# Kernel optimization log

Hardware: AMD Instinct MI355X
Metric: run time of the kernel (lower is better)

Reference implementation:

```python
import jax, jax.numpy as jnp
import numpy as np

BS, L, D, ITEM_NUM = 64, 100, 64, 100000  # batch, max_seq_len, embedding_dim, item vocab
NEG_INF = -10000.0


def setup_inputs() -> dict:
    key = jax.random.key(0)
    k1, k2, k3, k4, k5 = jax.random.split(key, 5)
    N = BS * (L + 1)
    return {
        "prec_vec": jax.random.normal(k1, (BS * L, D), jnp.float32),
        "score_embs": jax.random.normal(k2, (N, D), jnp.float32),
        "pop_prob_list": jax.random.uniform(k3, (ITEM_NUM + 1,), jnp.float32, 0.01, 1.0),
        "sample_items_id": jax.random.randint(k4, (N,), 0, ITEM_NUM + 1, dtype=jnp.int32),
        "log_mask": jax.random.randint(k5, (BS, L), 0, 2, dtype=jnp.int32),
    }


def reference(prec_vec, score_embs, pop_prob_list, sample_items_id, log_mask):
    bs, L_ = log_mask.shape
    N = sample_items_id.shape[0]  # bs * (L+1)

    # debiased in-batch sampled-softmax logits: [bs*L, N]
    debias = jnp.log(pop_prob_list[sample_items_id])
    logits = jnp.matmul(prec_vec, score_embs.T) - debias[None, :]

    # column mask: padded positions (log_mask==0); last position of each seq always valid
    col_valid = jnp.concatenate(
        [log_mask, jnp.ones((bs, 1), log_mask.dtype)], axis=1
    ).reshape(-1)  # [N]
    logits = jnp.where(col_valid[None, :] == 0, NEG_INF, logits)

    # duplicate-item mask: dup[i, k] = any item in sequence i equals sample_items_id[k]
    id_list = sample_items_id.reshape(bs, L_ + 1)
    dup = (sample_items_id[None, None, :] == id_list[:, :, None]).any(axis=1)  # [bs, N]

    # targets: label for (i, j) is flat column i*(L+1) + j + 1
    tgt = jnp.arange(bs)[:, None] * (L_ + 1) + jnp.arange(L_)[None, :] + 1  # [bs, L]

    # apply dup mask per (i, j) but never mask the row's own target column
    not_target = jnp.arange(N)[None, None, :] != tgt[:, :, None]  # [bs, L, N]
    mask3 = dup[:, None, :] & not_target
    logits3 = jnp.where(mask3, NEG_INF, logits.reshape(bs, L_, N))

    # masked cross-entropy, mean over valid (log_mask != 0) rows
    logits2 = logits3.reshape(bs * L_, N)
    labels = tgt.reshape(-1)
    logp = jax.nn.log_softmax(logits2, axis=-1)
    nll = -jnp.take_along_axis(logp, labels[:, None], axis=1)[:, 0]  # [bs*L]
    w = (log_mask.reshape(-1) != 0).astype(logits2.dtype)
    return jnp.sum(nll * w) / jnp.sum(w)
```

## Files before the change

kernel.cpp:

```cpp
#include <hip/hip_runtime.h>

#define NEG_INF (-10000.0f)
#define L_SEQ   100
#define N_COLS  6464
#define D_      64
#define N_ROWS  6400
#define NS      16

#define OFF_PS  0
#define OFF_XT  409600

typedef __attribute__((ext_vector_type(8))) short short8;
typedef __attribute__((ext_vector_type(4))) float f32x4;
union F8 { short8 v; unsigned short u[8]; unsigned w[4]; };

__device__ __forceinline__ unsigned short f2bf(float f) {
  unsigned u = __float_as_uint(f);
  return (unsigned short)((u + 0x7FFFu + ((u >> 16) & 1u)) >> 16);
}
__device__ __forceinline__ unsigned packbf(float lo, float hi) {
  return (__float_as_uint(hi) & 0xFFFF0000u) | (__float_as_uint(lo) >> 16);
}

__global__ __launch_bounds__(256, 4) void fused_kernel(
    const float* __restrict__ prec, const float* __restrict__ score,
    const float* __restrict__ pop, const int* __restrict__ sid,
    const int* __restrict__ lm,
    float* __restrict__ ps, float* __restrict__ xtrow) {
  __shared__ unsigned bs[2 * 3126];
  __shared__ unsigned short btile[64 * 64];
  __shared__ float mdl[2 * 64];

  const int tid = threadIdx.x;
  const int split = blockIdx.y;
  const int blkrow = blockIdx.x * 64;
  const int w = tid >> 6, lane = tid & 63;
  const int lr = lane & 15, lk = lane >> 4;
  const int rowbase = blkrow + w * 16;
  const int i0 = blkrow / L_SEQ;
  const int i1 = (blkrow + 63) / L_SEQ;
  const int lim = (i0 + 1) * L_SEQ;
  const int rbase4 = rowbase + lk * 4;

  for (int x = tid; x < 2 * 3126; x += 256) bs[x] = 0u;
  __syncthreads();
  if (tid < 202) {
    int sel = tid / 101, pos = tid - sel * 101;
    int iq = sel ? i1 : i0;
    int id = sid[iq * 101 + pos];
    atomicOr(&bs[sel * 3126 + (id >> 5)], 1u << (id & 31));
  }

  const float* prow = prec + (size_t)(rowbase + lr) * D_ + lk * 8;
  F8 fa0, fa1;
  {
    float4 a0 = *(const float4*)(prow);
    float4 a1 = *(const float4*)(prow + 4);
    float4 b0 = *(const float4*)(prow + 32);
    float4 b1 = *(const float4*)(prow + 36);
    fa0.u[0] = f2bf(a0.x); fa0.u[1] = f2bf(a0.y); fa0.u[2] = f2bf(a0.z); fa0.u[3] = f2bf(a0.w);
    fa0.u[4] = f2bf(a1.x); fa0.u[5] = f2bf(a1.y); fa0.u[6] = f2bf(a1.z); fa0.u[7] = f2bf(a1.w);
    fa1.u[0] = f2bf(b0.x); fa1.u[1] = f2bf(b0.y); fa1.u[2] = f2bf(b0.z); fa1.u[3] = f2bf(b0.w);
    fa1.u[4] = f2bf(b1.x); fa1.u[5] = f2bf(b1.y); fa1.u[6] = f2bf(b1.z); fa1.u[7] = f2bf(b1.w);
  }

  float s[4][4];
#pragma unroll
  for (int t4 = 0; t4 < 4; ++t4)
#pragma unroll
    for (int q = 0; q < 4; ++q) s[t4][q] = 0.f;

  float4 sv[4];
  int svN = 0, lmvN = 0;

  auto STAGE_ISSUE = [&](int stv) {
    const float* base = score + (size_t)stv * 64 * D_;
#pragma unroll
    for (int j = 0; j < 4; ++j)
      sv[j] = *(const float4*)(base + j * 1024 + tid * 4);
    if (tid < 64) {
      int c = stv * 64 + tid;
      svN = sid[c];
      int i2 = c / 101, p = c - i2 * 101;
      lmvN = (p == L_SEQ) ? 1 : lm[i2 * L_SEQ + p];
    }
  };
  auto STAGE_WRITE = [&]() {
#pragma unroll
    for (int j = 0; j < 4; ++j) {
      int colw = j * 16 + (tid >> 4);
      int byteoff = colw * 128 + ((((tid & 15) * 8)) ^ ((colw & 7) << 4));
      uint2 pk;
      pk.x = packbf(sv[j].x, sv[j].y);
      pk.y = packbf(sv[j].z, sv[j].w);
      *(uint2*)((char*)btile + byteoff) = pk;
    }
    if (tid < 64) {
      float inv = 1.0f / pop[svN];
      unsigned h0 = (bs[svN >> 5] >> (svN & 31)) & 1u;
      unsigned h1 = (bs[3126 + (svN >> 5)] >> (svN & 31)) & 1u;
      mdl[tid] = (lmvN && !h0) ? inv : 0.f;
      mdl[64 + tid] = (lmvN && !h1) ? inv : 0.f;
    }
  };
  auto COMPUTE = [&]() {
    const int sw = (lr & 7) << 4;
    F8 fb0[4], fb1[4];
    float ma[4], mb[4];
#pragma unroll
    for (int t4 = 0; t4 < 4; ++t4) {
      int col = t4 * 16 + lr;
      char* rowp = (char*)btile + col * 128;
      fb0[t4].v = *(const short8*)(rowp + ((lk * 16) ^ sw));
      fb1[t4].v = *(const short8*)(rowp + ((64 + lk * 16) ^ sw));
      ma[t4] = mdl[t4 * 16 + lr];
      mb[t4] = mdl[64 + t4 * 16 + lr];
    }
    f32x4 acc[4];
#pragma unroll
    for (int t4 = 0; t4 < 4; ++t4) {
      f32x4 z = {0.f, 0.f, 0.f, 0.f};
      z = __builtin_amdgcn_mfma_f32_16x16x32_bf16(fa0.v, fb0[t4].v, z, 0, 0, 0);
      z = __builtin_amdgcn_mfma_f32_16x16x32_bf16(fa1.v, fb1[t4].v, z, 0, 0, 0);
      acc[t4] = z;
    }
#pragma unroll
    for (int q = 0; q < 4; ++q) {
      const bool ub = (rbase4 + q) >= lim;
#pragma unroll
      for (int t4 = 0; t4 < 4; ++t4) {
        float mm = ub ? mb[t4] : ma[t4];
        s[t4][q] = fmaf(__expf(acc[t4][q]), mm, s[t4][q]);
      }
    }
  };

  const int nit = (100 - split) / NS + 1;
  int st = split;
  STAGE_ISSUE(st);
  __syncthreads();
  STAGE_WRITE();
  __syncthreads();
  for (int t = 0; t < nit; ++t) {
    const bool more = (t + 1 < nit);
    if (more) STAGE_ISSUE(st + NS);
    COMPUTE();
    if (more) {
      __syncthreads();
      STAGE_WRITE();
      __syncthreads();
    }
    st += NS;
  }

  float sq[4];
#pragma unroll
  for (int q = 0; q < 4; ++q)
    sq[q] = (s[0][q] + s[1][q]) + (s[2][q] + s[3][q]);
#pragma unroll
  for (int q = 0; q < 4; ++q) {
#pragma unroll
    for (int off = 1; off < 16; off <<= 1)
      sq[q] += __shfl_xor(sq[q], off);
  }
  if (lr == 0) {
#pragma unroll
    for (int q = 0; q < 4; ++q)
      ps[(size_t)(rbase4 + q) * NS + split] = sq[q];
  }

  if (split == 0) {
    int row_l = rowbase + lr;
    int i_l = row_l / L_SEQ, j_l = row_l - i_l * L_SEQ;
    int tgtc = i_l * 101 + j_l + 1;
    int p_l = j_l + 1;
    int vt = (p_l == L_SEQ) ? 1 : lm[i_l * L_SEQ + p_l];
    const float* srp = score + (size_t)tgtc * D_ + lk * 8;
    float4 s0 = *(const float4*)(srp);
    float4 s1 = *(const float4*)(srp + 4);
    float4 s2 = *(const float4*)(srp + 32);
    float4 s3 = *(const float4*)(srp + 36);
    F8 ft0, ft1;
    ft0.w[0] = packbf(s0.x, s0.y); ft0.w[1] = packbf(s0.z, s0.w);
    ft0.w[2] = packbf(s1.x, s1.y); ft0.w[3] = packbf(s1.z, s1.w);
    ft1.w[0] = packbf(s2.x, s2.y); ft1.w[1] = packbf(s2.z, s2.w);
    ft1.w[2] = packbf(s3.x, s3.y); ft1.w[3] = packbf(s3.z, s3.w);
    f32x4 z = {0.f, 0.f, 0.f, 0.f};
    z = __builtin_amdgcn_mfma_f32_16x16x32_bf16(fa0.v, ft0.v, z, 0, 0, 0);
    z = __builtin_amdgcn_mfma_f32_16x16x32_bf16(fa1.v, ft1.v, z, 0, 0, 0);
    int qs = lr - lk * 4;
    if (qs >= 0 && qs < 4) {
      float zd = (qs == 0) ? z[0] : (qs == 1) ? z[1] : (qs == 2) ? z[2] : z[3];
      float xv = zd - __logf(pop[sid[tgtc]]);
      xtrow[row_l] = vt ? xv : NEG_INF;
    }
  }
}

__global__ __launch_bounds__(1024) void merge_kernel(
    const float* __restrict__ ps, const float* __restrict__ xtrow,
    const int* __restrict__ lm, float* __restrict__ out) {
  float lsum = 0.f, lcnt = 0.f;
  for (int r = threadIdx.x; r < N_ROWS; r += 1024) {
    const float4* pp = (const float4*)(ps + (size_t)r * NS);
    float4 a = pp[0], b = pp[1], c = pp[2], d = pp[3];
    float sv = ((a.x + a.y) + (a.z + a.w)) + ((b.x + b.y) + (b.z + b.w)) +
               ((c.x + c.y) + (c.z + c.w)) + ((d.x + d.y) + (d.z + d.w));
    float x = xtrow[r];
    sv += __expf(x);
    sv = fmaxf(sv, 1e-37f);
    if (lm[r] != 0) { lsum += __logf(sv) - x; lcnt += 1.f; }
  }
#pragma unroll
  for (int off = 1; off < 64; off <<= 1) {
    lsum += __shfl_xor(lsum, off);
    lcnt += __shfl_xor(lcnt, off);
  }
  __shared__ float red[32];
  const int wid = threadIdx.x >> 6, lane = threadIdx.x & 63;
  if (lane == 0) { red[wid] = lsum; red[16 + wid] = lcnt; }
  __syncthreads();
  if (threadIdx.x == 0) {
    float S = 0.f, C = 0.f;
#pragma unroll
    for (int k = 0; k < 16; ++k) { S += red[k]; C += red[16 + k]; }
    out[0] = S / C;
  }
}

extern "C" void kernel_launch(void* const* d_in, const int* in_sizes, int n_in,
                              void* d_out, int out_size, void* d_ws, size_t ws_size,
                              hipStream_t stream) {
  const float* prec  = (const float*)d_in[0];
  const float* score = (const float*)d_in[1];
  const float* pop   = (const float*)d_in[2];
  const int*   sid   = (const int*)d_in[3];
  const int*   lm    = (const int*)d_in[4];

  char* ws = (char*)d_ws;
  float* ps    = (float*)(ws + OFF_PS);
  float* xtrow = (float*)(ws + OFF_XT);
  float* out   = (float*)d_out;

  hipLaunchKernelGGL(fused_kernel, dim3(100, NS), dim3(256), 0, stream,
                     prec, score, pop, sid, lm, ps, xtrow);
  hipLaunchKernelGGL(merge_kernel, dim3(1), dim3(1024), 0, stream,
                     ps, xtrow, lm, out);
}
```

Measured before the change: 34.14 us.

## Double-buffer score tiles, halve column splits, parallelize merge with atomics

The fused kernel now double-buffers the bf16 score tile and mask arrays in shared memory, so the next stage is written while the current one is read and one barrier per iteration is dropped. The column split count drops from 16 to 8, giving each block twice as many iterations, and the occupancy hint is lowered to 3 blocks. The single-block merge becomes 25 blocks that combine partial sums through atomics and a completion counter, at the cost of an extra memset launch and nondeterministic float accumulation order.

Measured after the change: 39.00 us. 14.2% more time.

```diff
diff --git a/kernel.cpp b/kernel.cpp
--- a/kernel.cpp
+++ b/kernel.cpp
@@ -5,10 +5,11 @@
 #define N_COLS  6464
 #define D_      64
 #define N_ROWS  6400
-#define NS      16
-
-#define OFF_PS  0
-#define OFF_XT  409600
+#define NS      8
+
+#define OFF_PS   0
+#define OFF_XT   204800
+#define OFF_ACC  230400
 
 typedef __attribute__((ext_vector_type(8))) short short8;
 typedef __attribute__((ext_vector_type(4))) float f32x4;
@@ -22,14 +23,14 @@
   return (__float_as_uint(hi) & 0xFFFF0000u) | (__float_as_uint(lo) >> 16);
 }
 
-__global__ __launch_bounds__(256, 4) void fused_kernel(
+__global__ __launch_bounds__(256, 3) void fused_kernel(
     const float* __restrict__ prec, const float* __restrict__ score,
     const float* __restrict__ pop, const int* __restrict__ sid,
     const int* __restrict__ lm,
     float* __restrict__ ps, float* __restrict__ xtrow) {
   __shared__ unsigned bs[2 * 3126];
-  __shared__ unsigned short btile[64 * 64];
-  __shared__ float mdl[2 * 64];
+  __shared__ unsigned short btile[2][64 * 64];
+  __shared__ float mdl[2][2 * 64];
 
   const int tid = threadIdx.x;
   const int split = blockIdx.y;
@@ -85,7 +86,7 @@
       lmvN = (p == L_SEQ) ? 1 : lm[i2 * L_SEQ + p];
     }
   };
-  auto STAGE_WRITE = [&]() {
+  auto STAGE_WRITE = [&](int buf) {
 #pragma unroll
     for (int j = 0; j < 4; ++j) {
       int colw = j * 16 + (tid >> 4);
@@ -93,28 +94,28 @@
       uint2 pk;
       pk.x = packbf(sv[j].x, sv[j].y);
       pk.y = packbf(sv[j].z, sv[j].w);
-      *(uint2*)((char*)btile + byteoff) = pk;
+      *(uint2*)((char*)btile[buf] + byteoff) = pk;
     }
     if (tid < 64) {
       float inv = 1.0f / pop[svN];
       unsigned h0 = (bs[svN >> 5] >> (svN & 31)) & 1u;
       unsigned h1 = (bs[3126 + (svN >> 5)] >> (svN & 31)) & 1u;
-      mdl[tid] = (lmvN && !h0) ? inv : 0.f;
-      mdl[64 + tid] = (lmvN && !h1) ? inv : 0.f;
+      mdl[buf][tid] = (lmvN && !h0) ? inv : 0.f;
+      mdl[buf][64 + tid] = (lmvN && !h1) ? inv : 0.f;
     }
   };
-  auto COMPUTE = [&]() {
+  auto COMPUTE = [&](int buf) {
     const int sw = (lr & 7) << 4;
     F8 fb0[4], fb1[4];
     float ma[4], mb[4];
 #pragma unroll
     for (int t4 = 0; t4 < 4; ++t4) {
       int col = t4 * 16 + lr;
-      char* rowp = (char*)btile + col * 128;
+      char* rowp = (char*)btile[buf] + col * 128;
       fb0[t4].v = *(const short8*)(rowp + ((lk * 16) ^ sw));
       fb1[t4].v = *(const short8*)(rowp + ((64 + lk * 16) ^ sw));
-      ma[t4] = mdl[t4 * 16 + lr];
-      mb[t4] = mdl[64 + t4 * 16 + lr];
+      ma[t4] = mdl[buf][t4 * 16 + lr];
+      mb[t4] = mdl[buf][64 + t4 * 16 + lr];
     }
     f32x4 acc[4];
 #pragma unroll
@@ -139,17 +140,18 @@
   int st = split;
   STAGE_ISSUE(st);
   __syncthreads();
-  STAGE_WRITE();
-  __syncthreads();
+  STAGE_WRITE(0);
+  __syncthreads();
+  int cur = 0;
   for (int t = 0; t < nit; ++t) {
     const bool more = (t + 1 < nit);
     if (more) STAGE_ISSUE(st + NS);
-    COMPUTE();
+    COMPUTE(cur);
     if (more) {
+      STAGE_WRITE(cur ^ 1);
       __syncthreads();
-      STAGE_WRITE();
-      __syncthreads();
-    }
+    }
+    cur ^= 1;
     st += NS;
   }
 
@@ -197,34 +199,41 @@
   }
 }
 
-__global__ __launch_bounds__(1024) void merge_kernel(
+__global__ __launch_bounds__(256) void merge_kernel(
     const float* __restrict__ ps, const float* __restrict__ xtrow,
-    const int* __restrict__ lm, float* __restrict__ out) {
-  float lsum = 0.f, lcnt = 0.f;
-  for (int r = threadIdx.x; r < N_ROWS; r += 1024) {
-    const float4* pp = (const float4*)(ps + (size_t)r * NS);
-    float4 a = pp[0], b = pp[1], c = pp[2], d = pp[3];
-    float sv = ((a.x + a.y) + (a.z + a.w)) + ((b.x + b.y) + (b.z + b.w)) +
-               ((c.x + c.y) + (c.z + c.w)) + ((d.x + d.y) + (d.z + d.w));
-    float x = xtrow[r];
-    sv += __expf(x);
-    sv = fmaxf(sv, 1e-37f);
-    if (lm[r] != 0) { lsum += __logf(sv) - x; lcnt += 1.f; }
-  }
+    const int* __restrict__ lm, float* __restrict__ acc,
+    unsigned* __restrict__ done, float* __restrict__ out) {
+  const int r = blockIdx.x * 256 + threadIdx.x;
+  const float4* pp = (const float4*)(ps + (size_t)r * NS);
+  float4 a = pp[0], b = pp[1];
+  float sv = ((a.x + a.y) + (a.z + a.w)) + ((b.x + b.y) + (b.z + b.w));
+  float x = xtrow[r];
+  sv += __expf(x);
+  sv = fmaxf(sv, 1e-37f);
+  const int v = (lm[r] != 0);
+  float nll = v ? (__logf(sv) - x) : 0.f;
+  float c = v ? 1.f : 0.f;
 #pragma unroll
   for (int off = 1; off < 64; off <<= 1) {
-    lsum += __shfl_xor(lsum, off);
-    lcnt += __shfl_xor(lcnt, off);
-  }
-  __shared__ float red[32];
-  const int wid = threadIdx.x >> 6, lane = threadIdx.x & 63;
-  if (lane == 0) { red[wid] = lsum; red[16 + wid] = lcnt; }
+    nll += __shfl_xor(nll, off);
+    c += __shfl_xor(c, off);
+  }
+  __shared__ float red[8];
+  const int wq = threadIdx.x >> 6, lane = threadIdx.x & 63;
+  if (lane == 0) { red[wq] = nll; red[4 + wq] = c; }
   __syncthreads();
   if (threadIdx.x == 0) {
-    float S = 0.f, C = 0.f;
-#pragma unroll
-    for (int k = 0; k < 16; ++k) { S += red[k]; C += red[16 + k]; }
-    out[0] = S / C;
+    float bsum = (red[0] + red[1]) + (red[2] + red[3]);
+    float bcnt = (red[4] + red[5]) + (red[6] + red[7]);
+    atomicAdd(&acc[0], bsum);
+    atomicAdd(&acc[1], bcnt);
+    __threadfence();
+    unsigned t = atomicAdd(done, 1u);
+    if (t == 24) {
+      float S = atomicAdd(&acc[0], 0.f);
+      float C = atomicAdd(&acc[1], 0.f);
+      out[0] = S / C;
+    }
   }
 }
 
@@ -238,12 +247,15 @@
   const int*   lm    = (const int*)d_in[4];
 
   char* ws = (char*)d_ws;
-  float* ps    = (float*)(ws + OFF_PS);
-  float* xtrow = (float*)(ws + OFF_XT);
-  float* out   = (float*)d_out;
-
+  float*    ps    = (float*)(ws + OFF_PS);
+  float*    xtrow = (float*)(ws + OFF_XT);
+  float*    acc   = (float*)(ws + OFF_ACC);
+  unsigned* done  = (unsigned*)(ws + OFF_ACC + 8);
+  float*    out   = (float*)d_out;
+
+  hipMemsetAsync(acc, 0, 12, stream);
   hipLaunchKernelGGL(fused_kernel, dim3(100, NS), dim3(256), 0, stream,
                      prec, score, pop, sid, lm, ps, xtrow);
-  hipLaunchKernelGGL(merge_kernel, dim3(1), dim3(1024), 0, stream,
-                     ps, xtrow, lm, out);
-}
+  hipLaunchKernelGGL(merge_kernel, dim3(25), dim3(256), 0, stream,
+                     ps, xtrow, lm, acc, done, out);
+}
```
